# Kernel optimization log

Measured on AMD Instinct MI355X. Metric: run time of the kernel, lower is better.

The kernel has to match this reference:

```python
import jax, jax.numpy as jnp
import numpy as np

B, S, D = 4, 4096, 1024

def setup_inputs() -> dict:
    key = jax.random.key(0)
    ks = jax.random.split(key, 7)
    s = 1.0 / np.sqrt(D)
    return {
        "x": jax.random.normal(ks[0], (B, S, D), dtype=jnp.float32),
        "Wq": jax.random.uniform(ks[1], (D, D), jnp.float32, -s, s),
        "bq": jax.random.uniform(ks[2], (D,), jnp.float32, -s, s),
        "Wk": jax.random.uniform(ks[3], (D, D), jnp.float32, -s, s),
        "bk": jax.random.uniform(ks[4], (D,), jnp.float32, -s, s),
        "Wv": jax.random.uniform(ks[5], (D, D), jnp.float32, -s, s),
        "bv": jax.random.uniform(ks[6], (D,), jnp.float32, -s, s),
    }

def reference(x, Wq, bq, Wk, bk, Wv, bv):
    # q/k/v projections: [B,S,D]
    q = jnp.einsum("bsd,ed->bse", x, Wq) + bq
    k = jnp.einsum("bsd,ed->bse", x, Wk) + bk
    v = jnp.einsum("bsd,ed->bse", x, Wv) + bv
    scale = jnp.asarray(x.shape[-1] ** 0.5, x.dtype)
    scores = jnp.einsum("bqd,bkd->bqk", q, k) / scale  # [B,S,S]
    probs = jax.nn.softmax(scores, axis=-1)
    return jnp.einsum("bqk,bkd->bqd", probs, v)
```

## Files before the change

kernel.cpp:

```cpp
#include <hip/hip_runtime.h>


typedef unsigned short u16;
typedef __attribute__((ext_vector_type(8))) short bf16x8;
typedef __attribute__((ext_vector_type(4))) float f32x4;

__device__ __forceinline__ float bf2f(u16 h) {
    unsigned int x = ((unsigned int)h) << 16;
    float f;
    __builtin_memcpy(&f, &x, 4);
    return f;
}

__device__ __forceinline__ u16 f2bf(float f) {
    unsigned int x;
    __builtin_memcpy(&x, &f, 4);
    unsigned int r = (x + 0x7FFFu + ((x >> 16) & 1u)) >> 16;
    return (u16)r;
}

__device__ __forceinline__ void load16_lds(const u16* g, u16* l) {
    __builtin_amdgcn_global_load_lds(
        (const __attribute__((address_space(1))) void*)g,
        (__attribute__((address_space(3))) void*)l, 16, 0, 0);
}

__global__ __launch_bounds__(256) void cvt_all(
    const float* __restrict__ x, const float* __restrict__ wq,
    const float* __restrict__ wk, const float* __restrict__ wv,
    u16* __restrict__ xo, u16* __restrict__ qo, u16* __restrict__ ko,
    u16* __restrict__ vo) {
    int i = blockIdx.x * 256 + threadIdx.x;
    const float* src;
    u16* dst;
    int idx;
    if (i < 4194304) {
        src = x; dst = xo; idx = i;
    } else {
        int j = i - 4194304;
        int sel = j >> 18;
        idx = j & 262143;
        src = (sel == 0) ? wq : (sel == 1) ? wk : wv;
        dst = (sel == 0) ? qo : (sel == 1) ? ko : vo;
    }
    float4 f = ((const float4*)src)[idx];
    ushort4 o;
    o.x = f2bf(f.x); o.y = f2bf(f.y); o.z = f2bf(f.z); o.w = f2bf(f.w);
    ((ushort4*)dst)[idx] = o;
}

__device__ __forceinline__ void mfma_core(
    const u16* __restrict__ A, const u16* __restrict__ B, int K, int ldA,
    int ldB, size_t rowA0, size_t rowB0, u16* As, u16* Bs, f32x4 acc[4][4]) {
    const int t = threadIdx.x;
    const int lane = t & 63;
    const int wave = t >> 6;
    const int wm = (wave >> 1) * 64;
    const int wn = (wave & 1) * 64;
    const int lm = lane & 15;
    const int qd = lane >> 4;
    const int kx = lm & 7;
    const int rl = lane >> 3;
    const int swz = ((lane & 7) ^ rl) << 3;

#pragma unroll
    for (int i = 0; i < 4; ++i)
#pragma unroll
        for (int j = 0; j < 4; ++j) acc[i][j] = (f32x4){0.f, 0.f, 0.f, 0.f};

    const u16* ga = A + (rowA0 + (size_t)(wave * 32 + rl)) * (size_t)ldA + swz;
    const u16* gb = B + (rowB0 + (size_t)(wave * 32 + rl)) * (size_t)ldB + swz;
    u16* la = As + wave * 2048;
    u16* lb = Bs + wave * 2048;

    for (int kb = 0; kb < K; kb += 64) {
#pragma unroll
        for (int p = 0; p < 4; ++p) {
            load16_lds(ga + (size_t)(p * 8) * ldA + kb, la + p * 512);
            load16_lds(gb + (size_t)(p * 8) * ldB + kb, lb + p * 512);
        }
        __syncthreads();
#pragma unroll
        for (int k0 = 0; k0 < 64; k0 += 32) {
            const int q0 = k0 >> 3;
            const int cofs = (((q0 + qd) ^ kx) << 3);
            bf16x8 a[4], b[4];
#pragma unroll
            for (int i = 0; i < 4; ++i) {
                a[i] = *(const bf16x8*)(As + (wm + i * 16 + lm) * 64 + cofs);
                b[i] = *(const bf16x8*)(Bs + (wn + i * 16 + lm) * 64 + cofs);
            }
#pragma unroll
            for (int i = 0; i < 4; ++i)
#pragma unroll
                for (int j = 0; j < 4; ++j)
                    acc[i][j] = __builtin_amdgcn_mfma_f32_16x16x32_bf16(
                        a[i], b[j], acc[i][j], 0, 0, 0);
        }
        __syncthreads();
    }
}

__global__ __launch_bounds__(256, 3) void proj_qkv(
    const u16* __restrict__ x, const u16* __restrict__ w0,
    const u16* __restrict__ w1, const u16* __restrict__ w2,
    const float* __restrict__ b0, const float* __restrict__ b1,
    const float* __restrict__ b2, u16* __restrict__ Qb, u16* __restrict__ Kb,
    u16* __restrict__ Vt) {
    __shared__ __align__(16) u16 As[128 * 64];
    __shared__ __align__(16) u16 Bs[128 * 64];
    const int z = blockIdx.z;
    const u16* W = (z == 0) ? w0 : (z == 1) ? w1 : w2;
    const float* bias = (z == 0) ? b0 : (z == 1) ? b1 : b2;

    const size_t rowA0 = (size_t)blockIdx.y * 128;
    const size_t rowB0 = (size_t)blockIdx.x * 128;
    f32x4 acc[4][4];
    mfma_core(x, W, 1024, 1024, 1024, rowA0, rowB0, As, Bs, acc);

    const int lane = threadIdx.x & 63;
    const int wave = threadIdx.x >> 6;
    const int wm = (wave >> 1) * 64;
    const int wn = (wave & 1) * 64;
    const int lm = lane & 15;
    const int qd = lane >> 4;

#pragma unroll
    for (int i = 0; i < 4; ++i) {
        const int r0 = (int)rowA0 + wm + i * 16 + qd * 4;
#pragma unroll
        for (int j = 0; j < 4; ++j) {
            const int col = (int)rowB0 + wn + j * 16 + lm;
            const float bv = bias[col];
            if (z < 2) {
                u16* C = z ? Kb : Qb;
#pragma unroll
                for (int r = 0; r < 4; ++r)
                    C[(size_t)(r0 + r) * 1024 + col] = f2bf(acc[i][j][r] + bv);
            } else {
                const int batch = r0 >> 12;
                const int s0 = r0 & 4095;
                ushort4 o;
                o.x = f2bf(acc[i][j][0] + bv);
                o.y = f2bf(acc[i][j][1] + bv);
                o.z = f2bf(acc[i][j][2] + bv);
                o.w = f2bf(acc[i][j][3] + bv);
                *(ushort4*)(Vt + (size_t)batch * 4194304 +
                            (size_t)col * 4096 + s0) = o;
            }
        }
    }
}

__global__ __launch_bounds__(256, 3) void gemm_scores(
    const u16* __restrict__ Qb, const u16* __restrict__ Kb,
    u16* __restrict__ SP, float* __restrict__ L) {
    __shared__ __align__(16) u16 As[128 * 64];
    __shared__ __align__(16) u16 Bs[128 * 64];
    __shared__ float Ls[256];
    const size_t z = blockIdx.z;
    const u16* A = Qb + z * 4194304;
    const u16* B = Kb + z * 4194304;
    u16* C = SP + z * 16777216;

    const size_t rowA0 = (size_t)blockIdx.y * 128;
    const size_t rowB0 = (size_t)blockIdx.x * 128;
    f32x4 acc[4][4];
    mfma_core(A, B, 1024, 1024, 1024, rowA0, rowB0, As, Bs, acc);

    const int lane = threadIdx.x & 63;
    const int wave = threadIdx.x >> 6;
    const int wm = (wave >> 1) * 64;
    const int wn = (wave & 1) * 64;
    const int lm = lane & 15;
    const int qd = lane >> 4;

#pragma unroll
    for (int i = 0; i < 4; ++i) {
        const int rl0 = wm + i * 16 + qd * 4;
        float part[4] = {0.f, 0.f, 0.f, 0.f};
#pragma unroll
        for (int j = 0; j < 4; ++j) {
            const int col = (int)rowB0 + wn + j * 16 + lm;
            u16 o[4];
#pragma unroll
            for (int r = 0; r < 4; ++r) {
                float e = __expf(acc[i][j][r] * 0.03125f);
                o[r] = f2bf(e);
                part[r] += e;
            }
#pragma unroll
            for (int r = 0; r < 4; ++r)
                C[(size_t)(rowA0 + rl0 + r) * 4096 + col] = o[r];
        }
#pragma unroll
        for (int r = 0; r < 4; ++r) {
#pragma unroll
            for (int o = 8; o >= 1; o >>= 1) part[r] += __shfl_xor(part[r], o);
        }
        if (lm == 0) {
#pragma unroll
            for (int r = 0; r < 4; ++r)
                Ls[(rl0 + r) * 2 + (wave & 1)] = part[r];
        }
    }
    __syncthreads();
    const int t = threadIdx.x;
    if (t < 128)
        atomicAdd(L + z * 4096 + rowA0 + t, Ls[t * 2] + Ls[t * 2 + 1]);
}

__global__ __launch_bounds__(256, 3) void gemm_pv(
    const u16* __restrict__ SP, const u16* __restrict__ Vt,
    float* __restrict__ out, const float* __restrict__ L) {
    __shared__ __align__(16) u16 As[128 * 64];
    __shared__ __align__(16) u16 Bs[128 * 64];
    const size_t z = blockIdx.z;
    const u16* A = SP + z * 16777216;
    const u16* B = Vt + z * 4194304;
    float* C = out + z * 4194304;

    const size_t rowA0 = (size_t)blockIdx.y * 128;
    const size_t rowB0 = (size_t)blockIdx.x * 128;
    f32x4 acc[4][4];
    mfma_core(A, B, 4096, 4096, 4096, rowA0, rowB0, As, Bs, acc);

    const int lane = threadIdx.x & 63;
    const int wave = threadIdx.x >> 6;
    const int wm = (wave >> 1) * 64;
    const int wn = (wave & 1) * 64;
    const int lm = lane & 15;
    const int qd = lane >> 4;

#pragma unroll
    for (int i = 0; i < 4; ++i) {
        const int r0 = (int)rowA0 + wm + i * 16 + qd * 4;
        float inv[4];
#pragma unroll
        for (int r = 0; r < 4; ++r) inv[r] = 1.0f / L[z * 4096 + r0 + r];
#pragma unroll
        for (int j = 0; j < 4; ++j) {
            const int col = (int)rowB0 + wn + j * 16 + lm;
#pragma unroll
            for (int r = 0; r < 4; ++r)
                C[(size_t)(r0 + r) * 1024 + col] = acc[i][j][r] * inv[r];
        }
    }
}

template <int MODE>
__global__ __launch_bounds__(256, 3) void gemm_nt(
    const u16* __restrict__ A, const u16* __restrict__ B,
    void* __restrict__ Cv, int K, int ldA, int ldB, int ldC, float scale) {
    __shared__ __align__(16) u16 As[128 * 64];
    __shared__ __align__(16) u16 Bs[128 * 64];
    const size_t rowA0 = (size_t)blockIdx.y * 128;
    const size_t rowB0 = (size_t)blockIdx.x * 128;
    f32x4 acc[4][4];
    mfma_core(A, B, K, ldA, ldB, rowA0, rowB0, As, Bs, acc);

    const int lane = threadIdx.x & 63;
    const int wave = threadIdx.x >> 6;
    const int wm = (wave >> 1) * 64;
    const int wn = (wave & 1) * 64;
    const int lm = lane & 15;
    const int qd = lane >> 4;

#pragma unroll
    for (int i = 0; i < 4; ++i) {
        const int r0 = (int)rowA0 + wm + i * 16 + qd * 4;
#pragma unroll
        for (int j = 0; j < 4; ++j) {
            const int col = (int)rowB0 + wn + j * 16 + lm;
            if (MODE == 2) {
                u16* C = (u16*)Cv;
#pragma unroll
                for (int r = 0; r < 4; ++r)
                    C[(size_t)(r0 + r) * ldC + col] = f2bf(acc[i][j][r] * scale);
            } else {
                float* C = (float*)Cv;
#pragma unroll
                for (int r = 0; r < 4; ++r)
                    C[(size_t)(r0 + r) * ldC + col] = acc[i][j][r];
            }
        }
    }
}

__global__ __launch_bounds__(256) void softmax_inplace(u16* __restrict__ P) {
    u16* p = P + (size_t)blockIdx.x * 4096;
    const int t = threadIdx.x;
    const int lane = t & 63;
    const int wave = t >> 6;
    __shared__ float redmax[4];
    __shared__ float redsum[4];

    uint4 raw0 = *(const uint4*)(p + t * 8);
    uint4 raw1 = *(const uint4*)(p + 2048 + t * 8);
    float v[16];
    {
        const u16* h0 = (const u16*)&raw0;
        const u16* h1 = (const u16*)&raw1;
#pragma unroll
        for (int i = 0; i < 8; ++i) v[i] = bf2f(h0[i]);
#pragma unroll
        for (int i = 0; i < 8; ++i) v[8 + i] = bf2f(h1[i]);
    }
    float m = v[0];
#pragma unroll
    for (int i = 1; i < 16; ++i) m = fmaxf(m, v[i]);
#pragma unroll
    for (int o = 32; o >= 1; o >>= 1) m = fmaxf(m, __shfl_xor(m, o));
    if (lane == 0) redmax[wave] = m;
    __syncthreads();
    m = fmaxf(fmaxf(redmax[0], redmax[1]), fmaxf(redmax[2], redmax[3]));

    float s = 0.f;
#pragma unroll
    for (int i = 0; i < 16; ++i) {
        v[i] = __expf(v[i] - m);
        s += v[i];
    }
#pragma unroll
    for (int o = 32; o >= 1; o >>= 1) s += __shfl_xor(s, o);
    if (lane == 0) redsum[wave] = s;
    __syncthreads();
    s = redsum[0] + redsum[1] + redsum[2] + redsum[3];
    const float inv = 1.0f / s;

    u16 ho[16];
#pragma unroll
    for (int i = 0; i < 16; ++i) ho[i] = f2bf(v[i] * inv);
    *(uint4*)(p + t * 8) = *(const uint4*)&ho[0];
    *(uint4*)(p + 2048 + t * 8) = *(const uint4*)&ho[8];
}

extern "C" void kernel_launch(void* const* d_in, const int* in_sizes, int n_in,
                              void* d_out, int out_size, void* d_ws, size_t ws_size,
                              hipStream_t stream) {
    const float* x  = (const float*)d_in[0];
    const float* Wq = (const float*)d_in[1];
    const float* bq = (const float*)d_in[2];
    const float* Wk = (const float*)d_in[3];
    const float* bk = (const float*)d_in[4];
    const float* Wv = (const float*)d_in[5];
    const float* bv = (const float*)d_in[6];
    float* out = (float*)d_out;

    const bool big = ws_size >= (size_t)234946560;
    char* w = (char*)d_ws;
    u16 *x_bf, *wq_bf, *wk_bf, *wv_bf, *Qb, *Kb, *Vt, *SP;
    float* L = nullptr;
    if (big) {
        SP    = (u16*)(w);
        x_bf  = (u16*)(w);
        wq_bf = (u16*)(w + 33554432);
        wk_bf = (u16*)(w + 35651584);
        wv_bf = (u16*)(w + 37748736);
        Qb    = (u16*)(w + 134217728);
        Kb    = (u16*)(w + 167772160);
        Vt    = (u16*)(w + 201326592);
        L     = (float*)(w + 234881024);
    } else {
        x_bf  = (u16*)(w);
        wq_bf = (u16*)(w + 33554432);
        wk_bf = (u16*)(w + 35651584);
        wv_bf = (u16*)(w + 37748736);
        Qb    = (u16*)(w + 39845888);
        Kb    = (u16*)(w + 73400320);
        Vt    = (u16*)(w + 106954752);
        SP    = (u16*)(w + 140509184);
    }

    cvt_all<<<19456, 256, 0, stream>>>(x, Wq, Wk, Wv, x_bf, wq_bf, wk_bf, wv_bf);

    proj_qkv<<<dim3(8, 128, 3), 256, 0, stream>>>(
        x_bf, wq_bf, wk_bf, wv_bf, bq, bk, bv, Qb, Kb, Vt);

    if (big) {
        hipMemsetAsync(L, 0, 16384 * sizeof(float), stream);
        gemm_scores<<<dim3(32, 32, 4), 256, 0, stream>>>(Qb, Kb, SP, L);
        gemm_pv<<<dim3(8, 32, 4), 256, 0, stream>>>(SP, Vt, out, L);
    } else {
        for (int b = 0; b < 4; ++b) {
            const size_t off = (size_t)b * 4194304;
            gemm_nt<2><<<dim3(32, 32, 1), 256, 0, stream>>>(
                Qb + off, Kb + off, SP, 1024, 1024, 1024, 4096, 0.03125f);
            softmax_inplace<<<4096, 256, 0, stream>>>(SP);
            gemm_nt<3><<<dim3(8, 32, 1), 256, 0, stream>>>(
                SP, Vt + off, out + off, 4096, 4096, 4096, 1024, 1.f);
        }
    }
}
```

Measured before the change: 579.4 us.

## Fold L zeroing into convert kernel, raise occupancy, swap grid axes

Removes the separate memset of the softmax row-sum buffer by having extra blocks of the convert kernel zero it. Raises the launch-bounds min-blocks hint from 3 to 4 on the projection, scores and PV GEMMs. Swaps the blockIdx x/y mapping in the scores and PV kernels so consecutive blocks share A rows (row tiles vary fastest), which changes L2 reuse. PV precomputes reciprocal row sums into shared memory once per block instead of each thread dividing. The higher occupancy hint may force register spills.

```diff
diff --git a/kernel.cpp b/kernel.cpp
--- a/kernel.cpp
+++ b/kernel.cpp
@@ -29,8 +29,12 @@
     const float* __restrict__ x, const float* __restrict__ wq,
     const float* __restrict__ wk, const float* __restrict__ wv,
     u16* __restrict__ xo, u16* __restrict__ qo, u16* __restrict__ ko,
-    u16* __restrict__ vo) {
+    u16* __restrict__ vo, float* __restrict__ L) {
     int i = blockIdx.x * 256 + threadIdx.x;
+    if (i >= 4980736) {
+        ((float4*)L)[i - 4980736] = (float4){0.f, 0.f, 0.f, 0.f};
+        return;
+    }
     const float* src;
     u16* dst;
     int idx;
@@ -101,7 +105,7 @@
     }
 }
 
-__global__ __launch_bounds__(256, 3) void proj_qkv(
+__global__ __launch_bounds__(256, 4) void proj_qkv(
     const u16* __restrict__ x, const u16* __restrict__ w0,
     const u16* __restrict__ w1, const u16* __restrict__ w2,
     const float* __restrict__ b0, const float* __restrict__ b1,
@@ -152,7 +156,7 @@
     }
 }
 
-__global__ __launch_bounds__(256, 3) void gemm_scores(
+__global__ __launch_bounds__(256, 4) void gemm_scores(
     const u16* __restrict__ Qb, const u16* __restrict__ Kb,
     u16* __restrict__ SP, float* __restrict__ L) {
     __shared__ __align__(16) u16 As[128 * 64];
@@ -163,8 +167,8 @@
     const u16* B = Kb + z * 4194304;
     u16* C = SP + z * 16777216;
 
-    const size_t rowA0 = (size_t)blockIdx.y * 128;
-    const size_t rowB0 = (size_t)blockIdx.x * 128;
+    const size_t rowA0 = (size_t)blockIdx.x * 128;
+    const size_t rowB0 = (size_t)blockIdx.y * 128;
     f32x4 acc[4][4];
     mfma_core(A, B, 1024, 1024, 1024, rowA0, rowB0, As, Bs, acc);
 
@@ -210,7 +214,7 @@
         atomicAdd(L + z * 4096 + rowA0 + t, Ls[t * 2] + Ls[t * 2 + 1]);
 }
 
-__global__ __launch_bounds__(256, 3) void gemm_pv(
+__global__ __launch_bounds__(256, 4) void gemm_pv(
     const u16* __restrict__ SP, const u16* __restrict__ Vt,
     float* __restrict__ out, const float* __restrict__ L) {
     __shared__ __align__(16) u16 As[128 * 64];
@@ -220,13 +224,18 @@
     const u16* B = Vt + z * 4194304;
     float* C = out + z * 4194304;
 
-    const size_t rowA0 = (size_t)blockIdx.y * 128;
-    const size_t rowB0 = (size_t)blockIdx.x * 128;
+    const size_t rowA0 = (size_t)blockIdx.x * 128;
+    const size_t rowB0 = (size_t)blockIdx.y * 128;
     f32x4 acc[4][4];
     mfma_core(A, B, 4096, 4096, 4096, rowA0, rowB0, As, Bs, acc);
 
-    const int lane = threadIdx.x & 63;
-    const int wave = threadIdx.x >> 6;
+    float* Lsh = (float*)As;
+    const int t = threadIdx.x;
+    if (t < 128) Lsh[t] = 1.0f / L[z * 4096 + rowA0 + t];
+    __syncthreads();
+
+    const int lane = t & 63;
+    const int wave = t >> 6;
     const int wm = (wave >> 1) * 64;
     const int wn = (wave & 1) * 64;
     const int lm = lane & 15;
@@ -234,16 +243,14 @@
 
 #pragma unroll
     for (int i = 0; i < 4; ++i) {
-        const int r0 = (int)rowA0 + wm + i * 16 + qd * 4;
-        float inv[4];
-#pragma unroll
-        for (int r = 0; r < 4; ++r) inv[r] = 1.0f / L[z * 4096 + r0 + r];
+        const int rl0 = wm + i * 16 + qd * 4;
+        const int r0 = (int)rowA0 + rl0;
 #pragma unroll
         for (int j = 0; j < 4; ++j) {
             const int col = (int)rowB0 + wn + j * 16 + lm;
 #pragma unroll
             for (int r = 0; r < 4; ++r)
-                C[(size_t)(r0 + r) * 1024 + col] = acc[i][j][r] * inv[r];
+                C[(size_t)(r0 + r) * 1024 + col] = acc[i][j][r] * Lsh[rl0 + r];
         }
     }
 }
@@ -372,15 +379,15 @@
         SP    = (u16*)(w + 140509184);
     }
 
-    cvt_all<<<19456, 256, 0, stream>>>(x, Wq, Wk, Wv, x_bf, wq_bf, wk_bf, wv_bf);
+    cvt_all<<<big ? 19472 : 19456, 256, 0, stream>>>(
+        x, Wq, Wk, Wv, x_bf, wq_bf, wk_bf, wv_bf, L);
 
     proj_qkv<<<dim3(8, 128, 3), 256, 0, stream>>>(
         x_bf, wq_bf, wk_bf, wv_bf, bq, bk, bv, Qb, Kb, Vt);
 
     if (big) {
-        hipMemsetAsync(L, 0, 16384 * sizeof(float), stream);
         gemm_scores<<<dim3(32, 32, 4), 256, 0, stream>>>(Qb, Kb, SP, L);
-        gemm_pv<<<dim3(8, 32, 4), 256, 0, stream>>>(SP, Vt, out, L);
+        gemm_pv<<<dim3(32, 8, 4), 256, 0, stream>>>(SP, Vt, out, L);
     } else {
         for (int b = 0; b < 4; ++b) {
             const size_t off = (size_t)b * 4194304;
```

Measured after the change: 528.2 us. -8.8%, faster.
